# Performance work log

Hardware: AMD Instinct MI355X
Metric: run time of the kernel (lower is better)

## Reference

```python
import jax, jax.numpy as jnp
import numpy as np

B, C_LIDAR, C_CAM = 2, 384, 80
H = W = 180
HW = H * W
HID, NCLS, P, NH, DFF, L, NMS_K = 128, 10, 200, 8, 256, 2, 3


def conv2d(x, w, b):
    y = jax.lax.conv_general_dilated(x, w, (1, 1), 'SAME', dimension_numbers=('NCHW', 'OIHW', 'NCHW'))
    return y + b[None, :, None, None]


def conv1d3(x, w, b):
    y = jax.lax.conv_general_dilated(x, w, (1,), 'SAME', dimension_numbers=('NCH', 'OIH', 'NCH'))
    return y + b[None, :, None]


def layer_norm(x, g, b, eps=1e-5):
    mu = jnp.mean(x, -1, keepdims=True)
    var = jnp.mean((x - mu) ** 2, -1, keepdims=True)
    return (x - mu) * jax.lax.rsqrt(var + eps) * g + b


def mha(q, k, v, wqkv, bqkv, wo, bo):
    Bq, Nq, C = q.shape
    dh = C // NH
    qh = (q @ wqkv[0].T + bqkv[0]).reshape(Bq, Nq, NH, dh)
    kh = (k @ wqkv[1].T + bqkv[1]).reshape(k.shape[0], -1, NH, dh)
    vh = (v @ wqkv[2].T + bqkv[2]).reshape(v.shape[0], -1, NH, dh)
    att = jax.nn.softmax(jnp.einsum('bqhd,bkhd->bhqk', qh, kh) * np.float32(1.0 / np.sqrt(dh)), axis=-1)
    out = jnp.einsum('bhqk,bkhd->bqhd', att, vh).reshape(Bq, Nq, C)
    return out @ wo.T + bo


def posembed(pos, w1, b1, g, bt, w2, b2):
    # Conv1d(2->C,k1) + BN(inference) + ReLU + Conv1d(C->C,k1); pos [B,N,2] -> [B,N,C]
    x = pos @ w1.T + b1
    x = jax.nn.relu(x * g + bt)
    return x @ w2.T + b2


def reference(lidar, cam, shared_w, shared_b, fused_w, fused_b, hm_w1, hm_b1, hm_g, hm_beta, hm_w2, hm_b2, ce_w, ce_b, pe_w1, pe_b1, pe_g, pe_beta, pe_w2, pe_b2, attn_wqkv, attn_bqkv, attn_wo, attn_bo, ln_g, ln_b, ffn_w1, ffn_b1, ffn_w2, ffn_b2, hc_w1, hc_b1, hc_g, hc_beta, hc_w2, hc_b2, hh_w1, hh_b1, hh_g, hh_beta, hh_w2, hh_b2):
    cam_feat = conv2d(cam, fused_w, fused_b)            # [B,HID,H,W]
    lidar_feat = conv2d(lidar, shared_w, shared_b)      # [B,HID,H,W]
    lidar_flat = lidar_feat.reshape(B, HID, HW)
    key_flat = cam_feat.reshape(B, HID, HW).transpose(0, 2, 1)   # [B,HW,HID]
    # heatmap head: ConvModule(conv+BN+ReLU) then conv -> classes
    h = jax.nn.relu(conv2d(lidar_feat, hm_w1, hm_b1) * hm_g[None, :, None, None] + hm_beta[None, :, None, None])
    dense_heatmap = conv2d(h, hm_w2, hm_b2)             # [B,NCLS,H,W]
    heatmap = jax.nn.sigmoid(jax.lax.stop_gradient(dense_heatmap))
    # max-pool local-max NMS
    pad = NMS_K // 2
    inner = jax.lax.reduce_window(heatmap, -jnp.inf, jax.lax.max, (1, 1, NMS_K, NMS_K), (1, 1, 1, 1), 'VALID')
    local_max = jnp.zeros_like(heatmap).at[:, :, pad:-pad, pad:-pad].set(inner)
    # nuScenes: classes 8,9 use kernel-size-1 pooling (identity)
    local_max = local_max.at[:, 8].set(heatmap[:, 8]).at[:, 9].set(heatmap[:, 9])
    heatmap = heatmap * (heatmap == local_max)
    # top-k proposals over flattened class*HW scores (== descending argsort[:P])
    _, top = jax.lax.top_k(heatmap.reshape(B, -1), P)
    top_cls = top // HW
    top_idx = top % HW
    qf = jnp.take_along_axis(lidar_flat, top_idx[:, None, :], axis=2)   # [B,HID,P]
    one_hot = jax.nn.one_hot(top_cls, NCLS, dtype=qf.dtype)             # [B,P,NCLS]
    qf = qf + (one_hot @ ce_w.T + ce_b).transpose(0, 2, 1)
    # BEV position grid (x/y cell centers, ij order matching HW flattening)
    gx = jnp.arange(H, dtype=qf.dtype) + 0.5
    gy = jnp.arange(W, dtype=qf.dtype) + 0.5
    bev = jnp.stack(jnp.meshgrid(gx, gy, indexing='ij'), -1).reshape(HW, 2)
    qpos = bev[top_idx]                                  # [B,P,2]
    x = qf.transpose(0, 2, 1)                            # [B,P,HID]
    for i in range(L):
        qpe = posembed(qpos, pe_w1[i, 0], pe_b1[i, 0], pe_g[i, 0], pe_beta[i, 0], pe_w2[i, 0], pe_b2[i, 0])
        kpe = posembed(bev[None], pe_w1[i, 1], pe_b1[i, 1], pe_g[i, 1], pe_beta[i, 1], pe_w2[i, 1], pe_b2[i, 1])
        k = key_flat + kpe
        sa = mha(x + qpe, x + qpe, x + qpe, attn_wqkv[i, 0], attn_bqkv[i, 0], attn_wo[i, 0], attn_bo[i, 0])
        x = layer_norm(x + sa, ln_g[i, 0], ln_b[i, 0])
        ca = mha(x + qpe, k, k, attn_wqkv[i, 1], attn_bqkv[i, 1], attn_wo[i, 1], attn_bo[i, 1])
        x = layer_norm(x + ca, ln_g[i, 1], ln_b[i, 1])
        f = jax.nn.relu(x @ ffn_w1[i].T + ffn_b1[i]) @ ffn_w2[i].T + ffn_b2[i]
        x = layer_norm(x + f, ln_g[i, 2], ln_b[i, 2])
        xc = x.transpose(0, 2, 1)                        # [B,HID,P]
        yc = jax.nn.relu(conv1d3(xc, hc_w1[i], hc_b1[i]) * hc_g[i][None, :, None] + hc_beta[i][None, :, None])
        center = conv1d3(yc, hc_w2[i], hc_b2[i]) + qpos.transpose(0, 2, 1)
        yh = jax.nn.relu(conv1d3(xc, hh_w1[i], hh_b1[i]) * hh_g[i][None, :, None] + hh_beta[i][None, :, None])
        hm_pred = conv1d3(yh, hh_w2[i], hh_b2[i])
        qpos = jax.lax.stop_gradient(center).transpose(0, 2, 1)   # .detach().clone().permute
    return jnp.concatenate([center, hm_pred], axis=1)   # [B, 2+NCLS, P]


def _n(key, i, shape, s=0.02):
    return s * jax.random.normal(jax.random.fold_in(key, i), shape, dtype=jnp.float32)


def setup_inputs():
    key = jax.random.key(0)
    z, o = jnp.zeros, jnp.ones
    return dict(
        lidar=jax.random.normal(jax.random.fold_in(key, 100), (B, C_LIDAR, H, W), dtype=jnp.float32),
        cam=jax.random.normal(jax.random.fold_in(key, 101), (B, C_CAM, H, W), dtype=jnp.float32),
        shared_w=_n(key, 0, (HID, C_LIDAR, 3, 3)), shared_b=z((HID,)),
        fused_w=_n(key, 1, (HID, C_CAM, 3, 3)), fused_b=z((HID,)),
        hm_w1=_n(key, 2, (HID, HID, 3, 3)), hm_b1=z((HID,)), hm_g=o((HID,)), hm_beta=z((HID,)),
        hm_w2=_n(key, 3, (NCLS, HID, 3, 3)), hm_b2=z((NCLS,)),
        ce_w=_n(key, 4, (HID, NCLS)), ce_b=z((HID,)),
        pe_w1=_n(key, 5, (L, 2, HID, 2), 0.1), pe_b1=z((L, 2, HID)),
        pe_g=o((L, 2, HID)), pe_beta=z((L, 2, HID)),
        pe_w2=_n(key, 6, (L, 2, HID, HID)), pe_b2=z((L, 2, HID)),
        attn_wqkv=_n(key, 7, (L, 2, 3, HID, HID), 0.05), attn_bqkv=z((L, 2, 3, HID)),
        attn_wo=_n(key, 8, (L, 2, HID, HID), 0.05), attn_bo=z((L, 2, HID)),
        ln_g=o((L, 3, HID)), ln_b=z((L, 3, HID)),
        ffn_w1=_n(key, 9, (L, DFF, HID)), ffn_b1=z((L, DFF)),
        ffn_w2=_n(key, 10, (L, HID, DFF)), ffn_b2=z((L, HID)),
        hc_w1=_n(key, 11, (L, HID, HID, 3)), hc_b1=z((L, HID)), hc_g=o((L, HID)), hc_beta=z((L, HID)),
        hc_w2=_n(key, 12, (L, 2, HID, 3)), hc_b2=z((L, 2)),
        hh_w1=_n(key, 13, (L, HID, HID, 3)), hh_b1=z((L, HID)), hh_g=o((L, HID)), hh_beta=z((L, HID)),
        hh_w2=_n(key, 14, (L, NCLS, HID, 3)), hh_b2=z((L, NCLS)),
    )
```

## Files before the change

kernel.cpp:

```cpp
#include <hip/hip_runtime.h>
#include <hip/hip_bf16.h>

typedef __hip_bfloat16 bf16;
typedef _Float16 f16;

#define HW 32400
#define NCLS 10
#define PQ 200
#define HIDDEN 128
#define NSPLIT 45
#define SPLITLEN 720
#define CHK 32
#define CAP 6144
#define NBIN 4096
#define L2E 1.44269504f

typedef __attribute__((ext_vector_type(8))) _Float16 half8;
typedef __attribute__((ext_vector_type(8))) short short8;
typedef __attribute__((ext_vector_type(4))) short short4v;
typedef __attribute__((ext_vector_type(4))) float f32x4;

__device__ __forceinline__ float b2f(bf16 v) { return __bfloat162float(v); }
__device__ __forceinline__ void stf(float* p, float v) { *p = v; }
__device__ __forceinline__ void stf(bf16* p, float v) { *p = __float2bfloat16(v); }
__device__ __forceinline__ float ldsel(const void* p, long i, unsigned isbf) {
  return isbf ? __bfloat162float(((const bf16*)p)[i]) : ((const float*)p)[i];
}
__device__ __forceinline__ float ldf(const float* p, long i) { return p[i]; }
__device__ __forceinline__ float ldf(const bf16* p, long i) { return __bfloat162float(p[i]); }
__device__ __forceinline__ short f2bf_bits(float v) {
  union { bf16 h; short s; } u; u.h = __float2bfloat16(v); return u.s;
}
__device__ __forceinline__ short f2h_bits(float v) {
  union { f16 h; short s; } u; u.h = (f16)v; return u.s;
}

__global__ void detect_k(const unsigned* __restrict__ L, unsigned* __restrict__ FLAGS)
{
  __shared__ unsigned cnt[2];
  int tid = threadIdx.x;
  if (tid < 2) cnt[tid] = 0;
  __syncthreads();
  unsigned nz = 0, pl = 0;
  for (int w = tid; w < 4096; w += 256) {
    unsigned u = L[w];
    if (u) {
      nz++;
      unsigned e = (u >> 7) & 0xFF;
      if (e >= 110 && e <= 140) pl++;
    }
  }
  atomicAdd(&cnt[0], nz);
  atomicAdd(&cnt[1], pl);
  __syncthreads();
  if (tid == 0) {
    FLAGS[0] = (2u * cnt[1] > cnt[0]) ? 1u : 0u;
    FLAGS[1] = 0u;
  }
}

struct CvtArgs { const void* src[40]; int n[40]; int off[40]; };
__global__ __launch_bounds__(256) void cvt_k(CvtArgs a, float* __restrict__ dst,
                                             const unsigned* __restrict__ FLAGS)
{
  int j = blockIdx.y;
  unsigned isbf = FLAGS[0];
  int n = a.n[j];
  const void* s = a.src[j];
  float* d = dst + a.off[j];
  for (int t = blockIdx.x * 256 + threadIdx.x; t < n; t += gridDim.x * 256)
    d[t] = ldsel(s, t, isbf);
}

__global__ __launch_bounds__(256) void wprep_k(const float* __restrict__ Wsrc,
    short* __restrict__ WB, int N, int K, int KB, int NTG, int split,
    const unsigned* __restrict__ FLAGS, int dynmode)
{
  unsigned isbf = dynmode ? FLAGS[0] : 0u;
  long total = (long)(split ? 2 : 1) * 9 * KB * NTG * 512;
  for (long t = (long)blockIdx.x * 256 + threadIdx.x; t < total;
       t += (long)gridDim.x * 256) {
    long r = t;
    int k = (int)(r & 31); r >>= 5;
    int n16 = (int)(r & 15); r >>= 4;
    int nt = (int)(r % NTG); r /= NTG;
    int kb = (int)(r % KB); r /= KB;
    int tap = (int)(r % 9); r /= 9;
    int plane = (int)r;
    int n = nt * 16 + n16, kk = kb * 32 + k;
    float v = 0.f;
    if (n < N && kk < K) v = Wsrc[((long)n * K + kk) * 9 + tap];
    short outv;
    if (isbf) {
      outv = (plane == 0) ? f2bf_bits(v) : (short)0;
    } else {
      f16 h = (f16)v;
      if (plane == 0) outv = f2h_bits((float)h);
      else outv = f2h_bits((v - (float)h) * 4096.0f);
    }
    WB[t] = outv;
  }
}

template <int MODE, int WM, int WN, int MT, int NT, int CW, typename CT>
__global__ __launch_bounds__(256) void conv_mfma(
    const void* __restrict__ A, const unsigned* __restrict__ FLAGS, int dyn,
    int gate, long abatch,
    const short* __restrict__ WB, const float* __restrict__ bias,
    const float* __restrict__ g, const float* __restrict__ beta, int act,
    CT* __restrict__ C, long cbatch, int N, int K, int KB, int NTG)
{
  constexpr int CPR = 180 / CW;
  constexpr int TOT = 180 * CPR;
  constexpr int BAND = (TOT + 7) / 8;
  constexpr int PXS = WM * MT * 16 + 2;
  constexpr int AW = 3 * PXS * 40;
  __shared__ __align__(16) short Ah[AW];
  __shared__ __align__(16) short Al[MODE == 3 ? AW : 8];
  if (gate >= 0 && FLAGS[0] != (unsigned)gate) return;
  int gsw = blockIdx.x;
  int idx = (gsw & 7) * BAND + (gsw >> 3);
  if (idx >= TOT) return;
  unsigned isbf = dyn ? FLAGS[0] : 0u;
  int bz = blockIdx.z;
  int y = idx / CPR;
  int x0 = (idx % CPR) * CW;
  int tid = threadIdx.x;
  int w = tid >> 6, lane = tid & 63;
  int lane15 = lane & 15, lgrp = lane >> 4;
  int wm = w % WM, wn = w / WM;
  int mbase = wm * MT * 16;
  int nbase = wn * NT * 16;
  f32x4 accM[MT][NT] = {};
  f32x4 accC[MODE == 3 ? MT : 1][MODE == 3 ? NT : 1] = {};
  long planeStride = (long)9 * KB * NTG * 512;

  for (int kb = 0; kb < KB; kb++) {
    __syncthreads();
    for (int u = tid; u < 3 * PXS * 4; u += 256) {
      int px = u % PXS;
      int t2 = u / PXS;
      int kg = t2 & 3, row = t2 >> 2;
      int gx = x0 + px - 1, gy = y + row - 1;
      bool in = (gx >= 0 && gx < 180 && gy >= 0 && gy < 180);
      long gbase = (long)bz * abatch + (long)(kb * 32 + kg * 8) * HW +
                   (long)gy * 180 + gx;
      short8 hv, lv;
#pragma unroll
      for (int j = 0; j < 8; j++) {
        int kk = kb * 32 + kg * 8 + j;
        if constexpr (MODE == 1) {
          hv[j] = (in && kk < K) ? ((const short*)A)[gbase + (long)j * HW]
                                 : (short)0;
        } else {
          float v = (in && kk < K) ? ldsel(A, gbase + (long)j * HW, isbf) : 0.f;
          f16 h = (f16)v;
          hv[j] = f2h_bits((float)h);
          if constexpr (MODE == 3) lv[j] = f2h_bits((v - (float)h) * 4096.0f);
        }
      }
      int o = (row * PXS + px) * 40 + kg * 8;
      *(short8*)&Ah[o] = hv;
      if constexpr (MODE == 3) *(short8*)&Al[o] = lv;
    }
    __syncthreads();
#pragma unroll
    for (int tap = 0; tap < 9; tap++) {
      int ty = tap / 3, tx = tap % 3;
      const short* wb = WB + (((long)tap * KB + kb) * NTG) * 512;
      if constexpr (MODE == 1) {
        short8 bh[NT];
#pragma unroll
        for (int nt = 0; nt < NT; nt++) {
          long o = (long)(wn * NT + nt) * 512 + lane15 * 32 + lgrp * 8;
          bh[nt] = *(const short8*)(wb + o);
        }
        short8 ah[MT];
#pragma unroll
        for (int mt = 0; mt < MT; mt++) {
          int px = mbase + mt * 16 + lane15 + tx;
          ah[mt] = *(const short8*)&Ah[(ty * PXS + px) * 40 + lgrp * 8];
        }
#pragma unroll
        for (int mt = 0; mt < MT; mt++)
#pragma unroll
          for (int nt = 0; nt < NT; nt++)
            accM[mt][nt] = __builtin_amdgcn_mfma_f32_16x16x32_bf16(
                ah[mt], bh[nt], accM[mt][nt], 0, 0, 0);
      } else {
        half8 bh[NT], bl[MODE == 3 ? NT : 1];
#pragma unroll
        for (int nt = 0; nt < NT; nt++) {
          long o = (long)(wn * NT + nt) * 512 + lane15 * 32 + lgrp * 8;
          bh[nt] = *(const half8*)(wb + o);
          if constexpr (MODE == 3) bl[nt] = *(const half8*)(wb + planeStride + o);
        }
        half8 ah[MT], al[MODE == 3 ? MT : 1];
#pragma unroll
        for (int mt = 0; mt < MT; mt++) {
          int px = mbase + mt * 16 + lane15 + tx;
          int o = (ty * PXS + px) * 40 + lgrp * 8;
          ah[mt] = *(const half8*)&Ah[o];
          if constexpr (MODE == 3) al[mt] = *(const half8*)&Al[o];
        }
#pragma unroll
        for (int mt = 0; mt < MT; mt++)
#pragma unroll
          for (int nt = 0; nt < NT; nt++) {
            accM[mt][nt] = __builtin_amdgcn_mfma_f32_16x16x32_f16(
                ah[mt], bh[nt], accM[mt][nt], 0, 0, 0);
            if constexpr (MODE == 3) {
              accC[mt][nt] = __builtin_amdgcn_mfma_f32_16x16x32_f16(
                  al[mt], bh[nt], accC[mt][nt], 0, 0, 0);
              accC[mt][nt] = __builtin_amdgcn_mfma_f32_16x16x32_f16(
                  ah[mt], bl[nt], accC[mt][nt], 0, 0, 0);
            }
          }
      }
    }
  }
  int pixbase = y * 180 + x0;
#pragma unroll
  for (int mt = 0; mt < MT; mt++) {
    int m = mbase + mt * 16 + lgrp * 4;
    if (m >= CW) continue;
#pragma unroll
    for (int nt = 0; nt < NT; nt++) {
      int n = nbase + nt * 16 + lane15;
      if (n >= N) continue;
      float bi = bias[n];
      float gg = g ? g[n] : 1.f;
      float bb = g ? beta[n] : 0.f;
      long base = (long)bz * cbatch + (long)n * HW + pixbase + m;
      float vv[4];
#pragma unroll
      for (int r = 0; r < 4; r++) {
        float v = accM[mt][nt][r];
        if constexpr (MODE == 3) v += accC[mt][nt][r] * (1.f / 4096.f);
        v += bi;
        if (g) v = v * gg + bb;
        if (act == 1) v = fmaxf(v, 0.f);
        else if (act == 2) v = 1.f / (1.f + expf(-v));
        vv[r] = v;
      }
      if constexpr (sizeof(CT) == 4) {
        if (m + 3 < CW) {
          f32x4 ov; ov[0] = vv[0]; ov[1] = vv[1]; ov[2] = vv[2]; ov[3] = vv[3];
          *(f32x4*)&C[base] = ov;
        } else {
#pragma unroll
          for (int r = 0; r < 4; r++) if (m + r < CW) C[base + r] = vv[r];
        }
      } else {
        if (m + 3 < CW) {
          short4v ov;
#pragma unroll
          for (int r = 0; r < 4; r++) ov[r] = f2bf_bits(vv[r]);
          *(short4v*)&C[base] = ov;
        } else {
#pragma unroll
          for (int r = 0; r < 4; r++)
            if (m + r < CW) *((short*)&C[base + r]) = f2bf_bits(vv[r]);
        }
      }
    }
  }
}

__global__ __launch_bounds__(256) void kvproj_k(
    const bf16* __restrict__ A1, const bf16* __restrict__ A2,
    const float* __restrict__ Wf, const float* __restrict__ bias,
    bf16* __restrict__ C)
{
  __shared__ __align__(16) short As[64 * 40];
  int m0 = blockIdx.x * 64;
  int n0 = blockIdx.y * 64;
  int b = blockIdx.z;
  int tid = threadIdx.x;
  int w = tid >> 6, lane = tid & 63;
  int lane15 = lane & 15, lgrp = lane >> 4;
  int wm = w & 1, wn = w >> 1;
  const bf16* A1b = A1 + (long)b * 128 * HW;
  f32x4 acc[2][2] = {};
  for (int kb = 0; kb < 4; kb++) {
    __syncthreads();
    for (int e = tid; e < 2048; e += 256) {
      int k = e >> 6, m = e & 63;
      int gm = m0 + m;
      float v = 0.f;
      if (gm < HW) {
        long idx = (long)(kb * 32 + k) * HW + gm;
        v = b2f(A1b[idx]) + b2f(A2[idx]);
      }
      As[m * 40 + k] = f2bf_bits(v);
    }
    __syncthreads();
    short8 bh[2];
#pragma unroll
    for (int nt = 0; nt < 2; nt++) {
      int n = n0 + wn * 32 + nt * 16 + lane15;
      const float* wr = Wf + (long)n * 128 + kb * 32 + lgrp * 8;
      float4 w0 = *(const float4*)wr;
      float4 w1 = *(const float4*)(wr + 4);
      short8 t;
      t[0] = f2bf_bits(w0.x); t[1] = f2bf_bits(w0.y);
      t[2] = f2bf_bits(w0.z); t[3] = f2bf_bits(w0.w);
      t[4] = f2bf_bits(w1.x); t[5] = f2bf_bits(w1.y);
      t[6] = f2bf_bits(w1.z); t[7] = f2bf_bits(w1.w);
      bh[nt] = t;
    }
    short8 ah[2];
#pragma unroll
    for (int mt = 0; mt < 2; mt++) {
      int m = wm * 32 + mt * 16 + lane15;
      ah[mt] = *(const short8*)&As[m * 40 + lgrp * 8];
    }
#pragma unroll
    for (int mt = 0; mt < 2; mt++)
#pragma unroll
      for (int nt = 0; nt < 2; nt++)
        acc[mt][nt] = __builtin_amdgcn_mfma_f32_16x16x32_bf16(
            ah[mt], bh[nt], acc[mt][nt], 0, 0, 0);
  }
#pragma unroll
  for (int mt = 0; mt < 2; mt++) {
    int mq = m0 + wm * 32 + mt * 16 + lgrp * 4;
    if (mq >= HW) continue;
#pragma unroll
    for (int nt = 0; nt < 2; nt++) {
      int n = n0 + wn * 32 + nt * 16 + lane15;
      float bi = bias[n];
      short4v ov;
#pragma unroll
      for (int r = 0; r < 4; r++) ov[r] = f2bf_bits(acc[mt][nt][r] + bi);
      *(short4v*)&C[(long)b * 256 * HW + (long)n * HW + mq] = ov;
    }
  }
}

template <typename AT, typename CT>
__global__ __launch_bounds__(256) void gemm_k(
    const AT* __restrict__ A, const AT* __restrict__ A2, int lda, int amode,
    long abatch,
    const float* __restrict__ W, const float* __restrict__ bias, int act,
    const float* __restrict__ res,
    const float* __restrict__ pe1w, const float* __restrict__ pe1b,
    const float* __restrict__ pe1g, const float* __restrict__ pe1bt,
    CT* __restrict__ C, int ldc, int cmode, long cbatch,
    int M, int N, int K)
{
  __shared__ __align__(16) float As[16][68];
  __shared__ __align__(16) float Ws[16][68];
  int b = blockIdx.z;
  int m0 = blockIdx.x * 64, n0 = blockIdx.y * 64;
  int tid = threadIdx.x;
  int nt = tid & 15, mt = tid >> 4;
  float acc[4][4] = {};
  const AT* Ab = A + (long)b * abatch;
  for (int k0 = 0; k0 < K; k0 += 16) {
    if (amode == 0) {
      for (int e = tid; e < 1024; e += 256) {
        int m = e >> 4, k = e & 15;
        float v = 0.f;
        if (m0 + m < M) {
          long idx = (long)(m0 + m) * lda + k0 + k;
          v = ldf(Ab, idx);
          if (A2) v += ldf(A2, idx);
        }
        As[k][m] = v;
      }
    } else if (amode == 2) {
      for (int e = tid; e < 1024; e += 256) {
        int m = e & 63, k = e >> 6;
        float v = 0.f;
        int gm = m0 + m;
        if (gm < M) {
          float p0 = (float)(gm / 180) + 0.5f;
          float p1 = (float)(gm % 180) + 0.5f;
          int kk = k0 + k;
          float t = p0 * pe1w[kk * 2] + p1 * pe1w[kk * 2 + 1] + pe1b[kk];
          t = t * pe1g[kk] + pe1bt[kk];
          v = fmaxf(t, 0.f);
        }
        As[k][m] = v;
      }
    } else {
      const float* qp = (const float*)A;
      for (int e = tid; e < 1024; e += 256) {
        int m = e & 63, k = e >> 6;
        float v = 0.f;
        int gm = m0 + m;
        if (gm < M) {
          float p0 = qp[gm * 2], p1 = qp[gm * 2 + 1];
          int kk = k0 + k;
          float t = p0 * pe1w[kk * 2] + p1 * pe1w[kk * 2 + 1] + pe1b[kk];
          t = t * pe1g[kk] + pe1bt[kk];
          v = fmaxf(t, 0.f);
        }
        As[k][m] = v;
      }
    }
    for (int e = tid; e < 1024; e += 256) {
      int n = e >> 4, k = e & 15;
      float v = 0.f;
      if (n0 + n < N) v = W[(long)(n0 + n) * K + k0 + k];
      Ws[k][n] = v;
    }
    __syncthreads();
#pragma unroll
    for (int kk = 0; kk < 16; kk++) {
      float4 av = *(const float4*)&As[kk][mt * 4];
      float4 wv = *(const float4*)&Ws[kk][nt * 4];
      float am[4] = {av.x, av.y, av.z, av.w};
      float wn[4] = {wv.x, wv.y, wv.z, wv.w};
#pragma unroll
      for (int mi = 0; mi < 4; mi++)
#pragma unroll
        for (int ni = 0; ni < 4; ni++)
          acc[mi][ni] = fmaf(am[mi], wn[ni], acc[mi][ni]);
    }
    __syncthreads();
  }
#pragma unroll
  for (int mi = 0; mi < 4; mi++) {
    int m = m0 + mt * 4 + mi;
    if (m >= M) continue;
#pragma unroll
    for (int ni = 0; ni < 4; ni++) {
      int n = n0 + nt * 4 + ni;
      if (n >= N) continue;
      float v = acc[mi][ni];
      if (bias) v += bias[n];
      if (act == 1) v = fmaxf(v, 0.f);
      if (res) v += res[(long)m * ldc + n];
      long ci = (cmode == 0) ? ((long)b * cbatch + (long)m * ldc + n)
                             : ((long)b * cbatch + (long)n * ldc + m);
      stf(&C[ci], v);
    }
  }
}

__global__ void nms_k(const float* __restrict__ HEAT, float* __restrict__ SCORE)
{
  int t = blockIdx.x * 256 + threadIdx.x;
  if (t >= 2 * NCLS * HW) return;
  int b = t / (NCLS * HW); int r = t % (NCLS * HW);
  int cls = r / HW; int n = r % HW;
  const float* hb = HEAT + ((long)(b * NCLS + cls)) * HW;
  float v = hb[n];
  bool keep = true;
  if (cls < 8) {
    int y = n / 180, x = n % 180;
    if (y == 0 || y == 179 || x == 0 || x == 179) keep = false;
    else {
      float mx = -1e30f;
#pragma unroll
      for (int dy = -1; dy <= 1; dy++)
#pragma unroll
        for (int dx = -1; dx <= 1; dx++)
          mx = fmaxf(mx, hb[(y + dy) * 180 + x + dx]);
      keep = (v == mx);
    }
  }
  SCORE[(long)b * (NCLS * HW) + r] = keep ? v : 0.f;
}

__global__ void zero_u32(unsigned* p, int n)
{
  int t = blockIdx.x * 256 + threadIdx.x;
  if (t < n) p[t] = 0;
}

__global__ __launch_bounds__(256) void hist_k(const float* __restrict__ SCORE,
                                              unsigned* __restrict__ HIST)
{
  __shared__ unsigned lh[NBIN];
  int b = blockIdx.y;
  for (int e = threadIdx.x; e < NBIN; e += 256) lh[e] = 0;
  __syncthreads();
  int start = blockIdx.x * 1350;
  const float* sb = SCORE + (long)b * (NCLS * HW);
  for (int e = start + threadIdx.x; e < start + 1350; e += 256) {
    unsigned bits = __float_as_uint(sb[e]);
    atomicAdd(&lh[bits >> 18], 1u);
  }
  __syncthreads();
  for (int e = threadIdx.x; e < NBIN; e += 256) {
    unsigned c = lh[e];
    if (c) atomicAdd(&HIST[b * NBIN + e], c);
  }
}

__global__ void thresh_k(const unsigned* __restrict__ HIST, unsigned* __restrict__ THR)
{
  __shared__ unsigned ps[256];
  int b = blockIdx.x;
  const unsigned* hb = HIST + b * NBIN;
  unsigned s = 0;
  for (int j = 0; j < 16; j++) s += hb[threadIdx.x * 16 + j];
  ps[threadIdx.x] = s;
  __syncthreads();
  if (threadIdx.x == 0) {
    unsigned cum = 0; int t = 255;
    for (; t > 0; t--) { if (cum + ps[t] >= PQ) break; cum += ps[t]; }
    int bin = t * 16 + 15;
    for (; bin > t * 16; bin--) { unsigned c = hb[bin]; if (cum + c >= PQ) break; cum += c; }
    if (bin < 1) bin = 1;
    THR[b] = (unsigned)bin;
  }
}

__global__ void collect_k(const float* __restrict__ SCORE, const unsigned* __restrict__ THR,
                          unsigned* __restrict__ ACNT, unsigned long long* __restrict__ CAND)
{
  int t = blockIdx.x * 256 + threadIdx.x;
  if (t >= 2 * NCLS * HW) return;
  int b = t / (NCLS * HW); int r = t % (NCLS * HW);
  float v = SCORE[(long)b * (NCLS * HW) + r];
  unsigned bits = __float_as_uint(v);
  if ((bits >> 18) >= THR[b]) {
    unsigned slot = atomicAdd(&ACNT[b], 1u);
    if (slot < CAP) CAND[(long)b * CAP + slot] =
        ((unsigned long long)bits << 32) | (unsigned)(~r);
  }
}

__global__ __launch_bounds__(64) void select_k(
    const unsigned long long* __restrict__ CAND, const unsigned* __restrict__ ACNT,
    unsigned* __restrict__ TOPC, unsigned* __restrict__ TOPI, float* __restrict__ QPA)
{
  __shared__ unsigned long long cnd[CAP];
  int b = blockIdx.x;
  int lane = threadIdx.x;
  unsigned cnt = ACNT[b]; if (cnt > CAP) cnt = CAP;
  for (int e = lane; e < (int)cnt; e += 64) cnd[e] = CAND[(long)b * CAP + e];
  __syncthreads();
  for (int p = 0; p < PQ; p++) {
    unsigned long long best = 0;
    for (int e = lane; e < (int)cnt; e += 64) { unsigned long long c = cnd[e]; if (c > best) best = c; }
#pragma unroll
    for (int o = 32; o; o >>= 1) {
      unsigned long long other = __shfl_xor(best, o, 64);
      if (other > best) best = other;
    }
    for (int e = lane; e < (int)cnt; e += 64) if (best != 0 && cnd[e] == best) cnd[e] = 0;
    if (lane == 0) {
      unsigned idx = (best == 0) ? 0u : ~(unsigned)(best & 0xFFFFFFFFull);
      if (idx >= NCLS * HW) idx = 0;
      unsigned cls = idx / HW, n = idx % HW;
      TOPC[b * PQ + p] = cls; TOPI[b * PQ + p] = n;
      QPA[((long)(b * PQ + p)) * 2 + 0] = (float)(n / 180) + 0.5f;
      QPA[((long)(b * PQ + p)) * 2 + 1] = (float)(n % 180) + 0.5f;
    }
    __syncthreads();
  }
}

__global__ void gather_k(const float* __restrict__ LIDF, const unsigned* __restrict__ TOPC,
                         const unsigned* __restrict__ TOPI, const float* __restrict__ cew,
                         const float* __restrict__ ceb, float* __restrict__ X)
{
  int t = blockIdx.x * 256 + threadIdx.x;
  if (t >= 2 * PQ * HIDDEN) return;
  int c = t & 127; int r = t >> 7; int p = r % PQ; int b = r / PQ;
  unsigned n = TOPI[b * PQ + p]; unsigned cls = TOPC[b * PQ + p];
  if (n >= HW) n = 0;
  if (cls >= NCLS) cls = 0;
  X[t] = LIDF[((long)(b * HIDDEN + c)) * HW + n] + cew[c * NCLS + cls] + ceb[c];
}

__global__ __launch_bounds__(64) void self_attn_k(const float* __restrict__ SQKV,
                                                  float* __restrict__ SAO)
{
  int q = blockIdx.x, h = blockIdx.y, b = blockIdx.z;
  int lane = threadIdx.x;
  const float* qp = SQKV + ((long)(b * PQ + q)) * 384 + h * 16;
  float qv[16];
#pragma unroll
  for (int d = 0; d < 16; d++) qv[d] = qp[d] * 0.25f;
  float sv[4]; int kks[4]; int nk = 0;
  float lmax = -1e30f;
  for (int kk = lane; kk < PQ; kk += 64) {
    const float* kp = SQKV + ((long)(b * PQ + kk)) * 384 + 128 + h * 16;
    float s = 0.f;
#pragma unroll
    for (int d = 0; d < 16; d++) s = fmaf(qv[d], kp[d], s);
    sv[nk] = s; kks[nk] = kk; nk++;
    lmax = fmaxf(lmax, s);
  }
#pragma unroll
  for (int o = 32; o; o >>= 1) lmax = fmaxf(lmax, __shfl_xor(lmax, o, 64));
  float lsum = 0.f; float acc[16] = {};
  for (int t = 0; t < nk; t++) {
    float p = expf(sv[t] - lmax);
    lsum += p;
    const float* vp = SQKV + ((long)(b * PQ + kks[t])) * 384 + 256 + h * 16;
#pragma unroll
    for (int d = 0; d < 16; d++) acc[d] = fmaf(p, vp[d], acc[d]);
  }
#pragma unroll
  for (int o = 32; o; o >>= 1) lsum += __shfl_xor(lsum, o, 64);
#pragma unroll
  for (int d = 0; d < 16; d++) {
    float v = acc[d];
#pragma unroll
    for (int o = 32; o; o >>= 1) v += __shfl_xor(v, o, 64);
    if (lane == 0) SAO[((long)(b * PQ + q)) * HIDDEN + h * 16 + d] = v / lsum;
  }
}

__global__ __launch_bounds__(256) void flash_mfma_k(const float* __restrict__ QH,
                                                    const bf16* __restrict__ KVT,
                                                    float* __restrict__ PART)
{
  __shared__ __align__(16) short Qs[64 * 40];
  __shared__ __align__(16) short Ks[2][32 * 40];
  __shared__ __align__(16) short Vs[2][16 * 40];
  __shared__ __align__(16) short Ps[4][16 * 40];
  int s = blockIdx.x, h = blockIdx.y;
  int b = blockIdx.z >> 2, qb = blockIdx.z & 3;
  int tid = threadIdx.x;
  int w = tid >> 6, lane = tid & 63;
  int lane15 = lane & 15, lgrp = lane >> 4;
  const short* Kb = (const short*)KVT + ((long)b * 256 + h * 16) * HW;
  const short* Vb = Kb + (long)128 * HW;
  int nbeg = s * SPLITLEN;

  for (int e = tid; e < 2 * 32 * 16; e += 256) {
    int buf = e >> 9, rr = e & 511;
    int kk = rr >> 4, d2 = rr & 15;
    Ks[buf][kk * 40 + 16 + d2] = 0;
  }
  {
    int q = tid >> 2, dg = tid & 3;
    int gq = qb * 64 + q;
    short8 v = {};
    if (dg < 2 && gq < PQ) {
      const float* qp = QH + ((long)(b * PQ + gq)) * HIDDEN + h * 16 + dg * 8;
#pragma unroll
      for (int j = 0; j < 8; j++) v[j] = f2bf_bits(qp[j] * 0.25f);
    }
    *(short8*)&Qs[q * 40 + dg * 8] = v;
  }

  auto stageKV = [&](int t, int buf) {
    int kb0 = nbeg + t * CHK;
    for (int e = tid; e < 512; e += 256) {
      int d = e >> 5, kk = e & 31;
      long gk = kb0 + kk; if (gk >= HW) gk = HW - 1;
      long go = (long)d * HW + gk;
      Ks[buf][kk * 40 + d] = Kb[go];
      Vs[buf][d * 40 + kk] = Vb[go];
    }
  };

  stageKV(0, 0);
  __syncthreads();

  short8 aq = *(const short8*)&Qs[(w * 16 + lane15) * 40 + lgrp * 8];
  float m[4] = {-1e30f, -1e30f, -1e30f, -1e30f};
  float l[4] = {0.f, 0.f, 0.f, 0.f};
  f32x4 accO = {};
  const int NTL = (SPLITLEN + CHK - 1) / CHK;
  for (int t = 0; t < NTL; t++) {
    int cur = t & 1;
    if (t + 1 < NTL) stageKV(t + 1, cur ^ 1);
    int valid = SPLITLEN - t * CHK; if (valid > CHK) valid = CHK;
    short8 bk0 = *(const short8*)&Ks[cur][lane15 * 40 + lgrp * 8];
    short8 bk1 = *(const short8*)&Ks[cur][(16 + lane15) * 40 + lgrp * 8];
    f32x4 z = {};
    f32x4 s0 = __builtin_amdgcn_mfma_f32_16x16x32_bf16(aq, bk0, z, 0, 0, 0);
    f32x4 s1 = __builtin_amdgcn_mfma_f32_16x16x32_bf16(aq, bk1, z, 0, 0, 0);
    bool msk0 = (lane15 >= valid);
    bool msk1 = (16 + lane15 >= valid);
#pragma unroll
    for (int r = 0; r < 4; r++) {
      float x0 = msk0 ? -1e30f : s0[r];
      float x1 = msk1 ? -1e30f : s1[r];
      float mx = fmaxf(x0, x1);
      mx = fmaxf(mx, __shfl_xor(mx, 1, 64));
      mx = fmaxf(mx, __shfl_xor(mx, 2, 64));
      mx = fmaxf(mx, __shfl_xor(mx, 4, 64));
      mx = fmaxf(mx, __shfl_xor(mx, 8, 64));
      float mn = fmaxf(m[r], mx);
      float p0 = exp2f((x0 - mn) * L2E);
      float p1 = exp2f((x1 - mn) * L2E);
      float sum = p0 + p1;
      sum += __shfl_xor(sum, 1, 64);
      sum += __shfl_xor(sum, 2, 64);
      sum += __shfl_xor(sum, 4, 64);
      sum += __shfl_xor(sum, 8, 64);
      float al = exp2f((m[r] - mn) * L2E);
      l[r] = l[r] * al + sum;
      m[r] = mn;
      accO[r] *= al;
      Ps[w][(lgrp * 4 + r) * 40 + lane15] = f2bf_bits(p0);
      Ps[w][(lgrp * 4 + r) * 40 + 16 + lane15] = f2bf_bits(p1);
    }
    short8 ap = *(const short8*)&Ps[w][lane15 * 40 + lgrp * 8];
    short8 bv = *(const short8*)&Vs[cur][lane15 * 40 + lgrp * 8];
    accO = __builtin_amdgcn_mfma_f32_16x16x32_bf16(ap, bv, accO, 0, 0, 0);
    __syncthreads();
  }
  long base = ((((long)(b * 8 + h)) * NSPLIT + s) * PQ) * 18;
#pragma unroll
  for (int r = 0; r < 4; r++) {
    int gq = qb * 64 + w * 16 + lgrp * 4 + r;
    if (gq < PQ) {
      long ro = base + (long)gq * 18;
      PART[ro + lane15] = accO[r];
      if (lane15 == 0) { PART[ro + 16] = m[r]; PART[ro + 17] = l[r]; }
    }
  }
}

__global__ void combine_k(const float* __restrict__ PART, float* __restrict__ CAO)
{
  int t = blockIdx.x * 256 + threadIdx.x;
  if (t >= 2 * 8 * PQ * 16) return;
  int d = t & 15; int r = t >> 4;
  int q = r % PQ; r /= PQ;
  int h = r & 7; int b = r >> 3;
  long base = (((long)(b * 8 + h)) * NSPLIT) * PQ * 18 + (long)q * 18;
  float M = -1e30f;
  for (int s = 0; s < NSPLIT; s++) M = fmaxf(M, PART[base + (long)s * PQ * 18 + 16]);
  float L = 0.f, O = 0.f;
  for (int s = 0; s < NSPLIT; s++) {
    long p0 = base + (long)s * PQ * 18;
    float w = expf(PART[p0 + 16] - M);
    L += PART[p0 + 17] * w;
    O += PART[p0 + d] * w;
  }
  CAO[((long)(b * PQ + q)) * HIDDEN + h * 16 + d] = (L > 0.f) ? O / L : 0.f;
}

__global__ __launch_bounds__(256) void ln_k(const float* __restrict__ PRE,
                                            const float* __restrict__ g,
                                            const float* __restrict__ bta,
                                            float* __restrict__ X)
{
  int row = blockIdx.x * 4 + (threadIdx.x >> 6);
  int lane = threadIdx.x & 63;
  const float* p = PRE + (long)row * HIDDEN;
  float v0 = p[lane], v1 = p[lane + 64];
  float s = v0 + v1;
#pragma unroll
  for (int o = 32; o; o >>= 1) s += __shfl_xor(s, o, 64);
  float mu = s * (1.f / 128.f);
  float d0 = v0 - mu, d1 = v1 - mu;
  float vs = d0 * d0 + d1 * d1;
#pragma unroll
  for (int o = 32; o; o >>= 1) vs += __shfl_xor(vs, o, 64);
  float rs = rsqrtf(vs * (1.f / 128.f) + 1e-5f);
  float* xo = X + (long)row * HIDDEN;
  xo[lane] = d0 * rs * g[lane] + bta[lane];
  xo[lane + 64] = d1 * rs * g[lane + 64] + bta[lane + 64];
}

__global__ __launch_bounds__(128) void conv1d_k(const float* __restrict__ X,
                                                const float* __restrict__ w,
                                                const float* __restrict__ bias,
                                                const float* __restrict__ g,
                                                const float* __restrict__ beta,
                                                float* __restrict__ Y)
{
  int p = blockIdx.x, b = blockIdx.y;
  int co = threadIdx.x;
  __shared__ float xs[3][HIDDEN];
  for (int e = co; e < 3 * HIDDEN; e += HIDDEN) {
    int t = e >> 7, c = e & 127;
    int pp = p + t - 1;
    xs[t][c] = (pp >= 0 && pp < PQ) ? X[((long)(b * PQ + pp)) * HIDDEN + c] : 0.f;
  }
  __syncthreads();
  const float* wr = w + (long)co * HIDDEN * 3;
  float acc = 0.f;
  for (int c = 0; c < HIDDEN; c++) {
    acc = fmaf(xs[0][c], wr[c * 3 + 0], acc);
    acc = fmaf(xs[1][c], wr[c * 3 + 1], acc);
    acc = fmaf(xs[2][c], wr[c * 3 + 2], acc);
  }
  float v = (acc + bias[co]) * g[co] + beta[co];
  Y[((long)(b * PQ + p)) * HIDDEN + co] = fmaxf(v, 0.f);
}

__global__ void head2_k(const float* __restrict__ Y, const float* __restrict__ w,
                        const float* __restrict__ bias, const float* __restrict__ qpos,
                        float* __restrict__ OUT, int N, float* __restrict__ qnext)
{
  int t = blockIdx.x * 256 + threadIdx.x;
  if (t >= 2 * N * PQ) return;
  int p = t % PQ; int r = t / PQ; int co = r % N; int b = r / N;
  const float* wr = w + (long)co * HIDDEN * 3;
  float acc = 0.f;
  for (int tap = 0; tap < 3; tap++) {
    int pp = p + tap - 1;
    if (pp < 0 || pp >= PQ) continue;
    const float* yr = Y + ((long)(b * PQ + pp)) * HIDDEN;
    for (int c = 0; c < HIDDEN; c++)
      acc = fmaf(yr[c], wr[c * 3 + tap], acc);
  }
  float v = acc + bias[co];
  if (qpos) v += qpos[((long)(b * PQ + p)) * 2 + co];
  OUT[((long)(b * N + co)) * PQ + p] = v;
  if (qnext) qnext[((long)(b * PQ + p)) * 2 + co] = v;
}

__global__ void out_k(const float* __restrict__ CENT, const float* __restrict__ HMP,
                      void* __restrict__ out, const unsigned* __restrict__ FLAGS)
{
  int t = blockIdx.x * 256 + threadIdx.x;
  if (t >= 2 * 12 * PQ) return;
  int p = t % PQ; int r = t / PQ; int ch = r % 12; int b = r / 12;
  float v = (ch < 2) ? CENT[((long)(b * 2 + ch)) * PQ + p]
                     : HMP[((long)(b * 10 + ch - 2)) * PQ + p];
  if (FLAGS[0]) ((bf16*)out)[t] = __float2bfloat16(v);
  else          ((float*)out)[t] = v;
}

extern "C" void kernel_launch(void* const* d_in, const int* in_sizes, int n_in,
                              void* d_out, int out_size, void* d_ws, size_t ws_size,
                              hipStream_t stream)
{
  (void)n_in; (void)out_size; (void)ws_size;

  float* F = (float*)d_ws;
  size_t off = 0;
  int aoff[42];
  {
    size_t acc = 0;
    for (int i = 2; i < 42; i++) { aoff[i] = (int)acc; acc += (size_t)in_sizes[i]; }
    off = acc;
  }
  float* ARENA = F;
  float* LIDF = F + off;
  bf16*  KVT16 = (bf16*)(F + off);
  off += 8294400;
  float* HBUF = F + off;
  bf16*  KPET16 = (bf16*)(F + off);
  float* PART  = F + off;
  off += 4147200;
  bf16*  CAMF16 = (bf16*)(F + off);
  off += 4147200;
  float* HEAT  = F + off;
  float* SCORE = F + off + 648000;
  off += 1296000;
  float* X   = F + off; off += 51200;
  float* XQ  = F + off; off += 51200;
  float* QPE = F + off; off += 51200;
  float* T1Q = F + off; off += 51200;
  float* SQKV = F + off; off += 153600;
  float* SAO = F + off; off += 51200;
  float* PRE = F + off; off += 51200;
  float* QH2 = F + off; off += 51200;
  float* CAO = F + off; off += 51200;
  float* FF1 = F + off; off += 102400;
  float* YC  = F + off; off += 51200;
  float* CENT = F + off; off += 800;
  float* HMP = F + off; off += 4000;
  float* QPA = F + off; off += 800;
  float* QPB = F + off; off += 800;
  unsigned* U = (unsigned*)(F + off);
  unsigned* HIST  = U;
  unsigned* ACNT  = U + 8192;
  unsigned* THR   = U + 8194;
  unsigned* FLAGS = U + 8196;
  unsigned* TOPC  = U + 8198;
  unsigned* TOPI  = U + 8598;
  unsigned long long* CAND = (unsigned long long*)(U + 9000);
  short* WB_LID = (short*)((((uintptr_t)X) + 15) & ~(uintptr_t)15);
  short* WB_CAM = WB_LID + 884736;
  short* WB_HM1 = WB_CAM + 110592;
  short* WB_HM2 = WB_HM1 + 294912;

  auto W = [&](int i) -> const float* { return ARENA + aoff[i]; };

  detect_k<<<1, 256, 0, stream>>>((const unsigned*)d_in[0], FLAGS);
  {
    CvtArgs a;
    for (int i = 2; i < 42; i++) { a.src[i - 2] = d_in[i]; a.n[i - 2] = in_sizes[i]; a.off[i - 2] = aoff[i]; }
    cvt_k<<<dim3(432, 40), 256, 0, stream>>>(a, ARENA, FLAGS);
  }
  wprep_k<<<3456, 256, 0, stream>>>(W(2), WB_LID, 128, 384, 12, 8, 1, FLAGS, 1);
  wprep_k<<<432, 256, 0, stream>>>(W(4), WB_CAM, 128, 80, 3, 8, 0, FLAGS, 1);
  wprep_k<<<1152, 256, 0, stream>>>(W(6), WB_HM1, 128, 128, 4, 8, 1, FLAGS, 0);
  wprep_k<<<144, 256, 0, stream>>>(W(10), WB_HM2, 10, 128, 4, 1, 1, FLAGS, 0);

  auto gemm = [&](const float* A, const float* A2, int lda, const float* Wp,
                  const float* bias, int act, const float* res, float* C, int ldc,
                  int M, int N, int K) {
    dim3 grid((M + 63) / 64, (N + 63) / 64, 1);
    gemm_k<float, float><<<grid, 256, 0, stream>>>(
        A, A2, lda, 0, 0L, Wp, bias, act, res,
        nullptr, nullptr, nullptr, nullptr, C, ldc, 0, 0L, M, N, K);
  };

  conv_mfma<1, 1, 4, 2, 2, 30, float><<<dim3(1080, 1, 2), 256, 0, stream>>>(
      d_in[0], FLAGS, 1, 1, (long)384 * HW, WB_LID, W(3), nullptr, nullptr, 0,
      LIDF, (long)128 * HW, 128, 384, 12, 8);
  conv_mfma<3, 1, 4, 2, 2, 30, float><<<dim3(1080, 1, 2), 256, 0, stream>>>(
      d_in[0], FLAGS, 1, 0, (long)384 * HW, WB_LID, W(3), nullptr, nullptr, 0,
      LIDF, (long)128 * HW, 128, 384, 12, 8);
  conv_mfma<1, 1, 4, 2, 2, 30, bf16><<<dim3(1080, 1, 2), 256, 0, stream>>>(
      d_in[1], FLAGS, 1, 1, (long)80 * HW, WB_CAM, W(5), nullptr, nullptr, 0,
      CAMF16, (long)128 * HW, 128, 80, 3, 8);
  conv_mfma<0, 1, 4, 2, 2, 30, bf16><<<dim3(1080, 1, 2), 256, 0, stream>>>(
      d_in[1], FLAGS, 1, 0, (long)80 * HW, WB_CAM, W(5), nullptr, nullptr, 0,
      CAMF16, (long)128 * HW, 128, 80, 3, 8);
  for (int b = 0; b < 2; b++) {
    conv_mfma<3, 1, 4, 2, 2, 30, float><<<dim3(1080, 1, 1), 256, 0, stream>>>(
        LIDF + (long)b * 128 * HW, FLAGS, 0, -1, 0L, WB_HM1, W(7), W(8), W(9), 1,
        HBUF, 0L, 128, 128, 4, 8);
    conv_mfma<3, 4, 1, 1, 1, 60, float><<<dim3(544, 1, 1), 256, 0, stream>>>(
        HBUF, FLAGS, 0, -1, 0L, WB_HM2, W(11), nullptr, nullptr, 2,
        HEAT + (long)b * NCLS * HW, 0L, 10, 128, 4, 1);
  }

  nms_k<<<(2 * NCLS * HW + 255) / 256, 256, 0, stream>>>(HEAT, SCORE);
  zero_u32<<<(8196 + 255) / 256, 256, 0, stream>>>(U, 8196);
  hist_k<<<dim3(240, 2), 256, 0, stream>>>(SCORE, HIST);
  thresh_k<<<2, 256, 0, stream>>>(HIST, THR);
  collect_k<<<(2 * NCLS * HW + 255) / 256, 256, 0, stream>>>(SCORE, THR, ACNT, CAND);
  select_k<<<2, 64, 0, stream>>>(CAND, ACNT, TOPC, TOPI, QPA);
  gather_k<<<200, 256, 0, stream>>>(LIDF, TOPC, TOPI, W(12), W(13), X);

  for (int i = 0; i < 2; i++) {
    const float* qcur = (i == 0) ? QPA : QPB;
    float* qnext = (i == 0) ? QPB : QPA;
    gemm_k<float, float><<<dim3(7, 2, 1), 256, 0, stream>>>(
        qcur, (const float*)nullptr, 0, 3, 0L,
        W(18) + (size_t)(i * 2 + 0) * 16384, W(19) + (i * 2 + 0) * 128, 0, nullptr,
        W(14) + (i * 2 + 0) * 256, W(15) + (i * 2 + 0) * 128,
        W(16) + (i * 2 + 0) * 128, W(17) + (i * 2 + 0) * 128,
        QPE, 128, 0, 0L, 400, 128, 128);
    gemm_k<float, bf16><<<dim3(507, 2, 1), 256, 0, stream>>>(
        ARENA, (const float*)nullptr, 0, 2, 0L,
        W(18) + (size_t)(i * 2 + 1) * 16384, W(19) + (i * 2 + 1) * 128, 0, nullptr,
        W(14) + (i * 2 + 1) * 256, W(15) + (i * 2 + 1) * 128,
        W(16) + (i * 2 + 1) * 128, W(17) + (i * 2 + 1) * 128,
        KPET16, HW, 1, 0L, 32400, 128, 128);
    gemm(X, QPE, 128, W(20) + (size_t)(i * 2 + 0) * 49152, W(21) + (i * 2 + 0) * 384,
         0, nullptr, SQKV, 384, 400, 384, 128);
    self_attn_k<<<dim3(200, 8, 2), 64, 0, stream>>>(SQKV, SAO);
    gemm(SAO, nullptr, 128, W(22) + (size_t)(i * 2 + 0) * 16384, W(23) + (i * 2 + 0) * 128,
         0, X, PRE, 128, 400, 128, 128);
    ln_k<<<100, 256, 0, stream>>>(PRE, W(24) + (i * 3 + 0) * 128, W(25) + (i * 3 + 0) * 128, X);
    gemm(X, QPE, 128, W(20) + (size_t)(i * 2 + 1) * 49152, W(21) + (i * 2 + 1) * 384,
         0, nullptr, QH2, 128, 400, 128, 128);
    kvproj_k<<<dim3(507, 4, 2), 256, 0, stream>>>(
        CAMF16, KPET16,
        W(20) + (size_t)(i * 2 + 1) * 49152 + 16384,
        W(21) + (i * 2 + 1) * 384 + 128, KVT16);
    flash_mfma_k<<<dim3(NSPLIT, 8, 8), 256, 0, stream>>>(QH2, KVT16, PART);
    combine_k<<<200, 256, 0, stream>>>(PART, CAO);
    gemm(CAO, nullptr, 128, W(22) + (size_t)(i * 2 + 1) * 16384, W(23) + (i * 2 + 1) * 128,
         0, X, PRE, 128, 400, 128, 128);
    ln_k<<<100, 256, 0, stream>>>(PRE, W(24) + (i * 3 + 1) * 128, W(25) + (i * 3 + 1) * 128, X);
    gemm(X, nullptr, 128, W(26) + (size_t)i * 32768, W(27) + i * 256,
         1, nullptr, FF1, 256, 400, 256, 128);
    gemm(FF1, nullptr, 256, W(28) + (size_t)i * 32768, W(29) + i * 128,
         0, X, PRE, 128, 400, 128, 256);
    ln_k<<<100, 256, 0, stream>>>(PRE, W(24) + (i * 3 + 2) * 128, W(25) + (i * 3 + 2) * 128, X);
    conv1d_k<<<dim3(200, 2), 128, 0, stream>>>(X, W(30) + (size_t)i * 49152,
        W(31) + i * 128, W(32) + i * 128, W(33) + i * 128, YC);
    head2_k<<<4, 256, 0, stream>>>(YC, W(34) + (size_t)i * 768, W(35) + i * 2,
        qcur, CENT, 2, qnext);
    conv1d_k<<<dim3(200, 2), 128, 0, stream>>>(X, W(36) + (size_t)i * 49152,
        W(37) + i * 128, W(38) + i * 128, W(39) + i * 128, YC);
    head2_k<<<16, 256, 0, stream>>>(YC, W(40) + (size_t)i * 3840, W(41) + i * 10,
        nullptr, HMP, 10, nullptr);
  }
  out_k<<<19, 256, 0, stream>>>(CENT, HMP, d_out, FLAGS);
}
```

Before: 2.023 ms.

## Prefetch next K-block into registers during MFMA and widen conv pixel tiles

The conv_mfma main loop now loads the next K-block's input tile from global memory into registers while the current block's MFMAs run, then writes it to LDS after a barrier. This is register-level software pipelining meant to hide global load latency. The big 3x3 convs also switch from 30-pixel to 60-pixel tiles (MT=4), halving the grid and increasing weight reuse per block. The cost is more registers for the prefetch buffers and larger accumulators, which may lower occupancy, especially in the split-precision MODE 3 path.

```diff
diff --git a/kernel.cpp b/kernel.cpp
--- a/kernel.cpp
+++ b/kernel.cpp
@@ -115,6 +115,8 @@
   constexpr int BAND = (TOT + 7) / 8;
   constexpr int PXS = WM * MT * 16 + 2;
   constexpr int AW = 3 * PXS * 40;
+  constexpr int UTOT = 3 * PXS * 4;
+  constexpr int NU = (UTOT + 255) / 256;
   __shared__ __align__(16) short Ah[AW];
   __shared__ __align__(16) short Al[MODE == 3 ? AW : 8];
   if (gate >= 0 && FLAGS[0] != (unsigned)gate) return;
@@ -135,35 +137,77 @@
   f32x4 accC[MODE == 3 ? MT : 1][MODE == 3 ? NT : 1] = {};
   long planeStride = (long)9 * KB * NTG * 512;
 
-  for (int kb = 0; kb < KB; kb++) {
-    __syncthreads();
-    for (int u = tid; u < 3 * PXS * 4; u += 256) {
-      int px = u % PXS;
-      int t2 = u / PXS;
-      int kg = t2 & 3, row = t2 >> 2;
-      int gx = x0 + px - 1, gy = y + row - 1;
-      bool in = (gx >= 0 && gx < 180 && gy >= 0 && gy < 180);
-      long gbase = (long)bz * abatch + (long)(kb * 32 + kg * 8) * HW +
-                   (long)gy * 180 + gx;
-      short8 hv, lv;
-#pragma unroll
-      for (int j = 0; j < 8; j++) {
-        int kk = kb * 32 + kg * 8 + j;
+  short8 preh[MODE == 1 ? NU : 1];
+  float pref[MODE == 1 ? 1 : NU][8];
+
+  auto issue = [&](int kb) {
+#pragma unroll
+    for (int iu = 0; iu < NU; iu++) {
+      int u = tid + iu * 256;
+      if (u < UTOT) {
+        int px = u % PXS;
+        int t2 = u / PXS;
+        int kg = t2 & 3, row = t2 >> 2;
+        int gx = x0 + px - 1, gy = y + row - 1;
+        bool in = (gx >= 0 && gx < 180 && gy >= 0 && gy < 180);
+        long gbase = (long)bz * abatch + (long)(kb * 32 + kg * 8) * HW +
+                     (long)gy * 180 + gx;
         if constexpr (MODE == 1) {
-          hv[j] = (in && kk < K) ? ((const short*)A)[gbase + (long)j * HW]
-                                 : (short)0;
+          short8 v = {};
+          if (in) {
+#pragma unroll
+            for (int j = 0; j < 8; j++) {
+              int kk = kb * 32 + kg * 8 + j;
+              v[j] = (kk < K) ? ((const short*)A)[gbase + (long)j * HW]
+                              : (short)0;
+            }
+          }
+          preh[iu] = v;
         } else {
-          float v = (in && kk < K) ? ldsel(A, gbase + (long)j * HW, isbf) : 0.f;
-          f16 h = (f16)v;
-          hv[j] = f2h_bits((float)h);
-          if constexpr (MODE == 3) lv[j] = f2h_bits((v - (float)h) * 4096.0f);
+#pragma unroll
+          for (int j = 0; j < 8; j++) {
+            int kk = kb * 32 + kg * 8 + j;
+            pref[iu][j] =
+                (in && kk < K) ? ldsel(A, gbase + (long)j * HW, isbf) : 0.f;
+          }
         }
       }
-      int o = (row * PXS + px) * 40 + kg * 8;
-      *(short8*)&Ah[o] = hv;
-      if constexpr (MODE == 3) *(short8*)&Al[o] = lv;
-    }
-    __syncthreads();
+    }
+  };
+
+  auto writeLDS = [&]() {
+#pragma unroll
+    for (int iu = 0; iu < NU; iu++) {
+      int u = tid + iu * 256;
+      if (u < UTOT) {
+        int px = u % PXS;
+        int t2 = u / PXS;
+        int kg = t2 & 3, row = t2 >> 2;
+        int o = (row * PXS + px) * 40 + kg * 8;
+        if constexpr (MODE == 1) {
+          *(short8*)&Ah[o] = preh[iu];
+        } else {
+          short8 hv, lv;
+#pragma unroll
+          for (int j = 0; j < 8; j++) {
+            float v = pref[iu][j];
+            f16 h = (f16)v;
+            hv[j] = f2h_bits((float)h);
+            if constexpr (MODE == 3) lv[j] = f2h_bits((v - (float)h) * 4096.0f);
+          }
+          *(short8*)&Ah[o] = hv;
+          if constexpr (MODE == 3) *(short8*)&Al[o] = lv;
+        }
+      }
+    }
+  };
+
+  issue(0);
+  writeLDS();
+  __syncthreads();
+
+  for (int kb = 0; kb < KB; kb++) {
+    if (kb + 1 < KB) issue(kb + 1);
 #pragma unroll
     for (int tap = 0; tap < 9; tap++) {
       int ty = tap / 3, tx = tap % 3;
@@ -218,7 +262,13 @@
           }
       }
     }
-  }
+    __syncthreads();
+    if (kb + 1 < KB) {
+      writeLDS();
+      __syncthreads();
+    }
+  }
+
   int pixbase = y * 180 + x0;
 #pragma unroll
   for (int mt = 0; mt < MT; mt++) {
@@ -895,20 +945,20 @@
         nullptr, nullptr, nullptr, nullptr, C, ldc, 0, 0L, M, N, K);
   };
 
-  conv_mfma<1, 1, 4, 2, 2, 30, float><<<dim3(1080, 1, 2), 256, 0, stream>>>(
+  conv_mfma<1, 1, 4, 4, 2, 60, float><<<dim3(544, 1, 2), 256, 0, stream>>>(
       d_in[0], FLAGS, 1, 1, (long)384 * HW, WB_LID, W(3), nullptr, nullptr, 0,
       LIDF, (long)128 * HW, 128, 384, 12, 8);
-  conv_mfma<3, 1, 4, 2, 2, 30, float><<<dim3(1080, 1, 2), 256, 0, stream>>>(
+  conv_mfma<3, 1, 4, 4, 2, 60, float><<<dim3(544, 1, 2), 256, 0, stream>>>(
       d_in[0], FLAGS, 1, 0, (long)384 * HW, WB_LID, W(3), nullptr, nullptr, 0,
       LIDF, (long)128 * HW, 128, 384, 12, 8);
-  conv_mfma<1, 1, 4, 2, 2, 30, bf16><<<dim3(1080, 1, 2), 256, 0, stream>>>(
+  conv_mfma<1, 1, 4, 4, 2, 60, bf16><<<dim3(544, 1, 2), 256, 0, stream>>>(
       d_in[1], FLAGS, 1, 1, (long)80 * HW, WB_CAM, W(5), nullptr, nullptr, 0,
       CAMF16, (long)128 * HW, 128, 80, 3, 8);
-  conv_mfma<0, 1, 4, 2, 2, 30, bf16><<<dim3(1080, 1, 2), 256, 0, stream>>>(
+  conv_mfma<0, 1, 4, 4, 2, 60, bf16><<<dim3(544, 1, 2), 256, 0, stream>>>(
       d_in[1], FLAGS, 1, 0, (long)80 * HW, WB_CAM, W(5), nullptr, nullptr, 0,
       CAMF16, (long)128 * HW, 128, 80, 3, 8);
   for (int b = 0; b < 2; b++) {
-    conv_mfma<3, 1, 4, 2, 2, 30, float><<<dim3(1080, 1, 1), 256, 0, stream>>>(
+    conv_mfma<3, 1, 4, 4, 2, 60, float><<<dim3(544, 1, 1), 256, 0, stream>>>(
         LIDF + (long)b * 128 * HW, FLAGS, 0, -1, 0L, WB_HM1, W(7), W(8), W(9), 1,
         HBUF, 0L, 128, 128, 4, 8);
     conv_mfma<3, 4, 1, 1, 1, 60, float><<<dim3(544, 1, 1), 256, 0, stream>>>(
```

New measurement: 2.534 ms. 25.3% more time.
